# Performance work log

Measured on AMD Instinct MI355X. Metric: run time of the kernel, lower is better.

## Reference

```python
import jax, jax.numpy as jnp
import numpy as np

HEADS = 16
EPS = 1e-5

def _ln(t):
    # LayerNorm over last axis, no affine params
    mu = jnp.mean(t, axis=-1, keepdims=True)
    var = jnp.var(t, axis=-1, keepdims=True)
    return (t - mu) / jnp.sqrt(var + EPS)

def setup_inputs() -> dict:
    key = jax.random.key(0)
    ks = jax.random.split(key, 8)
    b, n, dim, mlp_dim = 4, 2048, 1024, 4096
    s = lambda d: 1.0 / np.sqrt(d)
    return {
        "x": jax.random.normal(ks[0], (b, n, dim), dtype=jnp.float32),
        "Wqkv": jax.random.uniform(ks[1], (dim, 3 * dim), jnp.float32, -s(dim), s(dim)),
        "W1": jax.random.uniform(ks[2], (dim, mlp_dim), jnp.float32, -s(dim), s(dim)),
        "b1": jax.random.uniform(ks[3], (mlp_dim,), jnp.float32, -s(dim), s(dim)),
        "W2": jax.random.uniform(ks[4], (mlp_dim, dim), jnp.float32, -s(mlp_dim), s(mlp_dim)),
        "b2": jax.random.uniform(ks[5], (dim,), jnp.float32, -s(mlp_dim), s(mlp_dim)),
        "Wout": jax.random.uniform(ks[6], (dim, dim), jnp.float32, -s(dim), s(dim)),
        "bout": jax.random.uniform(ks[7], (dim,), jnp.float32, -s(dim), s(dim)),
    }

def reference(x, Wqkv, W1, b1, W2, b2, Wout, bout):
    b, n, dim = x.shape
    h = HEADS
    d = dim // h
    scale = dim ** (-0.5)  # NOTE: module scales by full dim, not head_dim
    qkv = x @ Wqkv  # [b, n, 3*dim]
    qkv = qkv.reshape(b, n, 3, h, d).transpose(2, 0, 3, 1, 4)  # [3, b, h, n, d]
    q, k, v = qkv[0], qkv[1], qkv[2]
    q, k = _ln(q), _ln(k)
    dots = jnp.einsum('bhid,bhjd->bhij', q, k) * scale
    attn = jax.nn.softmax(dots, axis=-1)
    attn_v = jnp.einsum('bhij,bhjd->bhid', attn, v)
    attn_v = attn_v.transpose(0, 2, 1, 3).reshape(b, n, dim)
    attn_out = attn_v @ Wout + bout
    parallel = jax.nn.gelu(x @ W1 + b1, approximate=False) @ W2 + b2
    return _ln(attn_out + parallel)
```

## Files before the change

### kernel.cpp

```cpp
#include <hip/hip_runtime.h>

typedef __attribute__((ext_vector_type(8))) short s16x8;
typedef __attribute__((ext_vector_type(4))) short s16x4;
typedef __attribute__((ext_vector_type(4))) float f32x4;
typedef __attribute__((ext_vector_type(16))) float f32x16;
typedef __attribute__((ext_vector_type(2))) unsigned uint2v;

#define DEVINL __device__ __forceinline__

DEVINL float b2f(short u){ return __uint_as_float(((unsigned)(unsigned short)u) << 16); }
DEVINL short f2bf(float f){
  unsigned u = __float_as_uint(f);
  u += 0x7fffu + ((u >> 16) & 1u);
  return (short)(u >> 16);
}
DEVINL unsigned cvtpk(float lo, float hi){
  unsigned r;
  asm("v_cvt_pk_bf16_f32 %0, %1, %2" : "=v"(r) : "v"(lo), "v"(hi));
  return r;
}
DEVINL float max3f(float a, float b, float c){
  float r; asm("v_max3_f32 %0, %1, %2, %3" : "=v"(r) : "v"(a), "v"(b), "v"(c)); return r;
}

#if __has_builtin(__builtin_amdgcn_exp2f)
#define EXP2F __builtin_amdgcn_exp2f
#else
#define EXP2F exp2f
#endif

DEVINL f32x4 mfma32(s16x8 a, s16x8 b, f32x4 c){
  return __builtin_amdgcn_mfma_f32_16x16x32_bf16(a, b, c, 0, 0, 0);
}
DEVINL f32x16 mfma3216(s16x8 a, s16x8 b, f32x16 c){
  return __builtin_amdgcn_mfma_f32_32x32x16_bf16(a, b, c, 0, 0, 0);
}

DEVINL uint2v pl32swap(unsigned a, unsigned b){
#if __has_builtin(__builtin_amdgcn_permlane32_swap)
  return __builtin_amdgcn_permlane32_swap(a, b, false, false);
#else
  asm volatile("v_permlane32_swap_b32 %0, %1" : "+v"(a), "+v"(b));
  uint2v r; r[0] = a; r[1] = b; return r;
#endif
}

typedef const unsigned __attribute__((address_space(1)))* gas1;
typedef unsigned __attribute__((address_space(3)))* las3;
DEVINL void gload16(const short* g, short* l){
  __builtin_amdgcn_global_load_lds((gas1)g, (las3)l, 16, 0, 0);
}

#define CFENCE asm volatile("" ::: "memory")
#define PBAR  do{ CFENCE; __builtin_amdgcn_sched_barrier(0); __builtin_amdgcn_s_barrier(); \
                  __builtin_amdgcn_sched_barrier(0); CFENCE; }while(0)
#define VMW8 asm volatile("s_waitcnt vmcnt(8)" ::: "memory")
#define VMW4 asm volatile("s_waitcnt vmcnt(4)" ::: "memory")
#define VMW0 asm volatile("s_waitcnt vmcnt(0)" ::: "memory")
#define PRIO1 __builtin_amdgcn_s_setprio(1)
#define PRIO0 __builtin_amdgcn_s_setprio(0)

static const int Bc   = 4;
static const int Nc   = 2048;
static const int DIM  = 1024;
static const int Tc   = Bc * Nc;
static const int MLP  = 4096;
static const int D3   = 3072;

static const size_t OFF_XB    = 0;
static const size_t OFF_WQKVT = OFF_XB    + 16777216;
static const size_t OFF_W1T   = OFF_WQKVT + 6291456;
static const size_t OFF_W2T   = OFF_W1T   + 8388608;
static const size_t OFF_WOUTT = OFF_W2T   + 8388608;
static const size_t OFF_QKV   = OFF_WOUTT + 2097152;
static const size_t OFF_QLN   = OFF_QKV   + 50331648;
static const size_t OFF_KLN   = OFF_QLN   + 16777216;
static const size_t OFF_VT    = OFF_KLN   + 16777216;
static const size_t OFF_ATTNV = OFF_VT    + 16777216;
static const size_t OFF_H     = OFF_QKV;
static const size_t OFF_S2    = OFF_KLN;

DEVINL void transp_body(const float* __restrict__ W, short* __restrict__ Wt,
                        int K, int N, int bid){
  __shared__ float tile[32][33];
  int ntx = N >> 5;
  int tx = bid % ntx, ty = bid / ntx;
  int r = threadIdx.x >> 3, c = (threadIdx.x & 7) * 4;
  f32x4 v = *(const f32x4*)(W + (size_t)(ty*32 + r)*N + tx*32 + c);
  tile[r][c] = v[0]; tile[r][c+1] = v[1]; tile[r][c+2] = v[2]; tile[r][c+3] = v[3];
  __syncthreads();
  s16x4 o;
#pragma unroll
  for (int j = 0; j < 4; ++j) o[j] = f2bf(tile[c+j][r]);
  *(s16x4*)(Wt + (size_t)(tx*32 + r)*K + ty*32 + c) = o;
}

__global__ __launch_bounds__(256) void prep_all(const float* __restrict__ x, short* __restrict__ xb,
                                                const float* __restrict__ Wqkv, short* __restrict__ wqkvt,
                                                const float* __restrict__ W1, short* __restrict__ w1t,
                                                const float* __restrict__ W2, short* __restrict__ w2t,
                                                const float* __restrict__ Wout, short* __restrict__ woutt){
  const int b = blockIdx.x;
  if (b < 4096){
    size_t i = ((size_t)b * 256 + threadIdx.x) * 8;
    f32x4 v0 = *(const f32x4*)(x + i);
    f32x4 v1 = *(const f32x4*)(x + i + 4);
    s16x8 o;
#pragma unroll
    for (int j = 0; j < 4; ++j){ o[j] = f2bf(v0[j]); o[4+j] = f2bf(v1[j]); }
    *(s16x8*)(xb + i) = o;
  } else if (b < 7168){
    transp_body(Wqkv, wqkvt, DIM, D3, b - 4096);
  } else if (b < 11264){
    transp_body(W1, w1t, DIM, MLP, b - 7168);
  } else if (b < 15360){
    transp_body(W2, w2t, MLP, DIM, b - 11264);
  } else {
    transp_body(Wout, woutt, DIM, DIM, b - 15360);
  }
}

template<int ACT, int FUSED, int QKVEPI>
__global__ __launch_bounds__(256, 2) void gemmCF(const short* __restrict__ A, const short* __restrict__ A2,
                                                 const short* __restrict__ Bt, const short* __restrict__ Bt2,
                                                 short* __restrict__ C,
                                                 const float* __restrict__ bias, const float* __restrict__ bias2,
                                                 int M, int N, int K1, int K2,
                                                 short* __restrict__ qln, short* __restrict__ kln,
                                                 short* __restrict__ vtb){
  __shared__ short lds[32768];

  const int tid = threadIdx.x;
  const int w = tid >> 6, lane = tid & 63;
  const int lr = lane & 15, g = lane >> 4;
  const int wr = w >> 1, wc = w & 1;
  const int NT1 = K1 >> 6;
  const int NT = NT1 + (FUSED ? (K2 >> 6) : 0);
  const int NIT = NT >> 1;

  const int nbn = N >> 7;
  const int cpx = gridDim.x >> 3;
  const int bid = (int)blockIdx.x;
  const int sw = (bid & 7)*cpx + (bid >> 3);
  const int nbn8 = nbn >> 3;
  const int T8 = sw >> 6, t64 = sw & 63;
  const int bm = (T8 / nbn8)*8 + (t64 >> 3);
  const int bn = (T8 % nbn8)*8 + (t64 & 7);

  const int l2 = lane >> 2;
  const int gsw = ((lane & 3) - ((lane >> 3) & 3)) & 3;
  const int cof = gsw * 8;
  const int qsw8 = ((g + (lr >> 1)) & 3) * 8;

  const short* ap0h = A  + (size_t)(bm*128 + w*16 + l2)*K1 + cof;
  const short* bp0h = Bt + (size_t)(bn*128 + w*16 + l2)*K1 + cof;
  const short* ap0a = FUSED ? (A2  + (size_t)(bm*128 + w*16 + l2)*K2 + cof) : nullptr;
  const short* bp0a = FUSED ? (Bt2 + (size_t)(bn*128 + w*16 + l2)*K2 + cof) : nullptr;

  auto stA = [&](int s, int T_, int kk){
    short* d0 = lds + s*4096 + w*512;
    if (FUSED && T_ >= NT1){
      size_t off = (size_t)(T_ - NT1)*64 + kk*32;
      gload16(ap0a + off, d0);
      gload16(ap0a + (size_t)64*K2 + off, d0 + 2048);
    } else {
      size_t off = (size_t)T_*64 + kk*32;
      gload16(ap0h + off, d0);
      gload16(ap0h + (size_t)64*K1 + off, d0 + 2048);
    }
  };
  auto stB = [&](int s, int T_, int kk){
    short* d0 = lds + 16384 + s*4096 + w*512;
    if (FUSED && T_ >= NT1){
      size_t off = (size_t)(T_ - NT1)*64 + kk*32;
      gload16(bp0a + off, d0);
      gload16(bp0a + (size_t)64*K2 + off, d0 + 2048);
    } else {
      size_t off = (size_t)T_*64 + kk*32;
      gload16(bp0h + off, d0);
      gload16(bp0h + (size_t)64*K1 + off, d0 + 2048);
    }
  };

#define LDA(s, mi) (*(const s16x8*)&lds[(s)*4096 + (wr*64 + (mi)*16 + lr)*32 + qsw8])
#define LDB(s, ni) (*(const s16x8*)&lds[16384 + (s)*4096 + (wc*64 + (ni)*16 + lr)*32 + qsw8])

  f32x4 acc[4][4] = {};
#define MM(ai, r) \
  acc[r][0]=mfma32(ai,b0,acc[r][0]); acc[r][1]=mfma32(ai,b1,acc[r][1]); \
  acc[r][2]=mfma32(ai,b2,acc[r][2]); acc[r][3]=mfma32(ai,b3,acc[r][3]);
#define RD(s) s16x8 a0=LDA(s,0),a1=LDA(s,1),a2=LDA(s,2),a3=LDA(s,3), \
                    b0=LDB(s,0),b1=LDB(s,1),b2=LDB(s,2),b3=LDB(s,3);
#define MM16 MM(a0,0) MM(a1,1) MM(a2,2) MM(a3,3)

  stA(0,0,0); stB(0,0,0);
  stA(1,0,1); stB(1,0,1);
  stA(2,1,0); stB(2,1,0);
  VMW8;
  PBAR;

  for (int i = 0; i < NIT; ++i){
    const int t = i << 1;
    const bool more = (i + 1 < NIT);
    {
      RD(0)
      stA(3, t+1, 1); stB(3, t+1, 1);
      PBAR; PRIO1; MM16 PRIO0;
      VMW8;
      PBAR;
    }
    {
      RD(1)
      if (more){ stA(0, t+2, 0); stB(0, t+2, 0); }
      PBAR; PRIO1; MM16 PRIO0;
      if (more){ VMW8; } else { VMW4; }
      PBAR;
    }
    {
      RD(2)
      if (more){ stA(1, t+2, 1); stB(1, t+2, 1); }
      PBAR; PRIO1; MM16 PRIO0;
      if (more){ VMW8; } else { VMW0; }
      PBAR;
    }
    {
      RD(3)
      if (more){ stA(2, t+3, 0); stB(2, t+3, 0); }
      PBAR; PRIO1; MM16 PRIO0;
      if (more){ VMW8; }
      PBAR;
    }
  }
#undef MM
#undef RD
#undef MM16
#undef LDA
#undef LDB

  if constexpr (QKVEPI){
#pragma unroll
    for (int a = 0; a < 4; ++a){
#pragma unroll
      for (int ni = 0; ni < 4; ++ni){
        const int col = wc*64 + ni*16 + lr;
        f32x4 v = acc[a][ni];
#pragma unroll
        for (int ii = 0; ii < 4; ++ii)
          lds[(wr*64 + a*16 + 4*g + ii)*130 + col] = f2bf(v[ii]);
      }
    }
    __syncthreads();
    const int part = (bn*128) >> 10;
    const int h0 = ((bn*128) & 1023) >> 6;
    const int rg = bm*128;
    const int b = rg >> 11;
    const int tok0 = rg & 2047;

    if (part < 2){
      short* dstbase = part ? kln : qln;
      const float sc = part ? 1.f : 0.04508422003f;
      const int row = tid >> 1, grp = tid & 1;
      const short* src = &lds[row*130 + grp*64];
      float s = 0.f, sq = 0.f;
#pragma unroll
      for (int i2 = 0; i2 < 8; ++i2){
        s16x8 u = *(const s16x8*)(src + i2*8);
#pragma unroll
        for (int j = 0; j < 8; ++j){ float fv = b2f(u[j]); s += fv; sq += fv*fv; }
      }
      const float mu = s * (1.f/64.f);
      const float var = sq * (1.f/64.f) - mu*mu;
      const float inv = rsqrtf(var + 1e-5f) * sc;
      const int bh = b*16 + h0 + grp;
      short* dst = dstbase + ((size_t)bh*Nc + tok0 + row)*64;
#pragma unroll
      for (int i2 = 0; i2 < 8; ++i2){
        s16x8 u = *(const s16x8*)(src + i2*8);
        s16x8 o;
#pragma unroll
        for (int j = 0; j < 8; ++j) o[j] = f2bf((b2f(u[j]) - mu) * inv);
        *(s16x8*)(dst + i2*8) = o;
      }
    } else {
      const int d = tid & 63, hh = (tid >> 6) & 1, half = tid >> 7;
      const int bh = b*16 + h0 + hh;
      short* dst = vtb + ((size_t)bh*64 + d)*Nc + tok0 + half*64;
#pragma unroll
      for (int i2 = 0; i2 < 8; ++i2){
        s16x8 o;
#pragma unroll
        for (int j = 0; j < 8; ++j)
          o[j] = lds[(half*64 + i2*8 + j)*130 + hh*64 + d];
        *(s16x8*)(dst + i2*8) = o;
      }
    }
    return;
  }

#pragma unroll
  for (int a = 0; a < 4; ++a){
#pragma unroll
    for (int ni = 0; ni < 4; ++ni){
      const int col = wc*64 + ni*16 + lr;
      float bv = bias ? bias[bn*128 + col] : 0.f;
      if (FUSED && bias2) bv += bias2[bn*128 + col];
      f32x4 v = acc[a][ni];
#pragma unroll
      for (int ii = 0; ii < 4; ++ii){
        float val = v[ii] + bv;
        if constexpr (ACT) val = 0.5f*val*(1.f + erff(val*0.70710678118f));
        lds[(wr*64 + a*16 + 4*g + ii)*128 + col] = f2bf(val);
      }
    }
  }
  __syncthreads();
  const size_t crow0 = (size_t)bm * 128;
  const int ch = (tid & 15) * 8;
#pragma unroll
  for (int p = 0; p < 8; ++p){
    const int row = p*16 + (tid >> 4);
    *(s16x8*)&C[(crow0 + row)*N + bn*128 + ch] = *(const s16x8*)&lds[row*128 + ch];
  }
}

__global__ __launch_bounds__(256) void attn_kern(const short* __restrict__ qln, const short* __restrict__ kln,
                                                 const short* __restrict__ vtb, short* __restrict__ attnv){
  __shared__ short Ks[2][64*72];
  __shared__ short Vs[2][64*72];
  const int tid = threadIdx.x;
  const int bh = blockIdx.x >> 4, qt = blockIdx.x & 15;
  const int b = bh >> 4, h = bh & 15;
  const int w = tid >> 6, lane = tid & 63;
  const int lq = lane & 31, hi = lane >> 5;
  const int qrow = qt*128 + w*32 + lq;

  const short* qp = qln + ((size_t)bh*Nc + qrow)*64 + hi*8;
  s16x8 qf[4];
#pragma unroll
  for (int m = 0; m < 4; ++m) qf[m] = *(const s16x8*)(qp + m*16);

  f32x16 o0 = {0,0,0,0,0,0,0,0,0,0,0,0,0,0,0,0};
  f32x16 o1 = {0,0,0,0,0,0,0,0,0,0,0,0,0,0,0,0};
  float mrun = -INFINITY, l = 0.f;

  const int sr = tid >> 3;
  const int sc = (tid & 7) * 8;
  const short* kb0 = kln + (size_t)bh*Nc*64;
  const short* vb0 = vtb + (size_t)bh*64*Nc;

  s16x8 kr0, kr1, vr0, vr1;
  {
    kr0 = *(const s16x8*)(kb0 + (size_t)sr*64 + sc);
    kr1 = *(const s16x8*)(kb0 + (size_t)(32 + sr)*64 + sc);
    vr0 = *(const s16x8*)(vb0 + (size_t)sr*Nc + sc);
    vr1 = *(const s16x8*)(vb0 + (size_t)(32 + sr)*Nc + sc);
  }

  for (int kt = 0; kt < 32; ++kt){
    const int cur = kt & 1;
    *(s16x8*)&Ks[cur][sr*72 + sc]        = kr0;
    *(s16x8*)&Ks[cur][(32 + sr)*72 + sc] = kr1;
    *(s16x8*)&Vs[cur][sr*72 + sc]        = vr0;
    *(s16x8*)&Vs[cur][(32 + sr)*72 + sc] = vr1;
    __syncthreads();
    if (kt + 1 < 32){
      const short* kb = kb0 + (size_t)(kt+1)*64*64;
      const short* vb = vb0 + (kt+1)*64;
      kr0 = *(const s16x8*)(kb + (size_t)sr*64 + sc);
      kr1 = *(const s16x8*)(kb + (size_t)(32 + sr)*64 + sc);
      vr0 = *(const s16x8*)(vb + (size_t)sr*Nc + sc);
      vr1 = *(const s16x8*)(vb + (size_t)(32 + sr)*Nc + sc);
    }

    f32x16 st0 = {0,0,0,0,0,0,0,0,0,0,0,0,0,0,0,0};
    f32x16 st1 = {0,0,0,0,0,0,0,0,0,0,0,0,0,0,0,0};
#pragma unroll
    for (int m = 0; m < 4; ++m){
      s16x8 kf0 = *(const s16x8*)&Ks[cur][ lq      *72 + m*16 + hi*8];
      s16x8 kf1 = *(const s16x8*)&Ks[cur][(32 + lq)*72 + m*16 + hi*8];
      st0 = mfma3216(kf0, qf[m], st0);
      st1 = mfma3216(kf1, qf[m], st1);
    }

    float cmax = max3f(st0[0], st0[1], st0[2]);
    cmax = max3f(cmax, st0[3], st0[4]);   cmax = max3f(cmax, st0[5], st0[6]);
    cmax = max3f(cmax, st0[7], st0[8]);   cmax = max3f(cmax, st0[9], st0[10]);
    cmax = max3f(cmax, st0[11], st0[12]); cmax = max3f(cmax, st0[13], st0[14]);
    cmax = max3f(cmax, st0[15], st1[0]);  cmax = max3f(cmax, st1[1], st1[2]);
    cmax = max3f(cmax, st1[3], st1[4]);   cmax = max3f(cmax, st1[5], st1[6]);
    cmax = max3f(cmax, st1[7], st1[8]);   cmax = max3f(cmax, st1[9], st1[10]);
    cmax = max3f(cmax, st1[11], st1[12]); cmax = max3f(cmax, st1[13], st1[14]);
    cmax = fmaxf(cmax, st1[15]);
    cmax = fmaxf(cmax, __shfl_xor(cmax, 32));
    if (__any(cmax > mrun + 8.f)){
      float mnew = fmaxf(mrun, cmax);
      float fr = EXP2F(mrun - mnew);
      l *= fr;
#pragma unroll
      for (int r = 0; r < 16; ++r){ o0[r] *= fr; o1[r] *= fr; }
      mrun = mnew;
    }
    float p0[16], p1[16];
#pragma unroll
    for (int r = 0; r < 16; ++r){
      p0[r] = EXP2F(st0[r] - mrun); l += p0[r];
      p1[r] = EXP2F(st1[r] - mrun); l += p1[r];
    }

#pragma unroll
    for (int kc = 0; kc < 2; ++kc){
      const float* p = kc ? p1 : p0;
#pragma unroll
      for (int kh = 0; kh < 2; ++kh){
        int r0 = kh*8;
        unsigned wa = cvtpk(p[r0+0], p[r0+1]);
        unsigned wb = cvtpk(p[r0+4], p[r0+5]);
        unsigned wc2 = cvtpk(p[r0+2], p[r0+3]);
        unsigned wd = cvtpk(p[r0+6], p[r0+7]);
        uint2v s1 = pl32swap(wa, wb);
        uint2v s2 = pl32swap(wc2, wd);
        union { unsigned u[4]; s16x8 v; } pu;
        pu.u[0] = s1[0]; pu.u[1] = s2[0]; pu.u[2] = s1[1]; pu.u[3] = s2[1];
        s16x8 vf0 = *(const s16x8*)&Vs[cur][ lq      *72 + kc*32 + kh*16 + hi*8];
        s16x8 vf1 = *(const s16x8*)&Vs[cur][(32 + lq)*72 + kc*32 + kh*16 + hi*8];
        o0 = mfma3216(vf0, pu.v, o0);
        o1 = mfma3216(vf1, pu.v, o1);
      }
    }
  }

  l += __shfl_xor(l, 32);
  float inv = 1.f / l;
  short* orow = attnv + ((size_t)(b*Nc + qrow))*DIM + h*64;
#pragma unroll
  for (int r = 0; r < 16; r += 2){
    int dv = (r&3) + 8*(r>>2) + 4*hi;
    *(unsigned*)&orow[dv]      = cvtpk(o0[r]*inv, o0[r+1]*inv);
    *(unsigned*)&orow[32 + dv] = cvtpk(o1[r]*inv, o1[r+1]*inv);
  }
}

__global__ __launch_bounds__(256) void final_ln(const short* __restrict__ s2, float* __restrict__ out){
  __shared__ float red[16];
  int row = blockIdx.x, tid = threadIdx.x;
  size_t base = (size_t)row*DIM + tid*4;
  s16x4 a = *(const s16x4*)(s2 + base);
  float v[4]; float s = 0.f, sq = 0.f;
#pragma unroll
  for (int i = 0; i < 4; ++i){ v[i] = b2f(a[i]); s += v[i]; sq += v[i]*v[i]; }
#pragma unroll
  for (int m = 1; m < 64; m <<= 1){ s += __shfl_xor(s, m); sq += __shfl_xor(sq, m); }
  int wv = tid >> 6;
  if ((tid & 63) == 0){ red[wv] = s; red[8 + wv] = sq; }
  __syncthreads();
  if (tid == 0){
    float S = red[0] + red[1] + red[2] + red[3];
    float Q = red[8] + red[9] + red[10] + red[11];
    float mu = S * (1.f/1024.f);
    float var = Q * (1.f/1024.f) - mu*mu;
    red[12] = mu; red[13] = rsqrtf(var + 1e-5f);
  }
  __syncthreads();
  float mu = red[12], inv = red[13];
#pragma unroll
  for (int i = 0; i < 4; ++i) out[base + i] = (v[i] - mu) * inv;
}

extern "C" void kernel_launch(void* const* d_in, const int* in_sizes, int n_in,
                              void* d_out, int out_size, void* d_ws, size_t ws_size,
                              hipStream_t stream){
  const float* x    = (const float*)d_in[0];
  const float* Wqkv = (const float*)d_in[1];
  const float* W1   = (const float*)d_in[2];
  const float* b1   = (const float*)d_in[3];
  const float* W2   = (const float*)d_in[4];
  const float* b2   = (const float*)d_in[5];
  const float* Wout = (const float*)d_in[6];
  const float* bout = (const float*)d_in[7];
  float* out = (float*)d_out;
  char* ws = (char*)d_ws;

  short* xb    = (short*)(ws + OFF_XB);
  short* wqkvt = (short*)(ws + OFF_WQKVT);
  short* w1t   = (short*)(ws + OFF_W1T);
  short* w2t   = (short*)(ws + OFF_W2T);
  short* woutt = (short*)(ws + OFF_WOUTT);
  short* qln   = (short*)(ws + OFF_QLN);
  short* kln   = (short*)(ws + OFF_KLN);
  short* vtb   = (short*)(ws + OFF_VT);
  short* attnv = (short*)(ws + OFF_ATTNV);
  short* hbuf  = (short*)(ws + OFF_H);
  short* s2    = (short*)(ws + OFF_S2);

  prep_all<<<16384, 256, 0, stream>>>(x, xb, Wqkv, wqkvt, W1, w1t, W2, w2t, Wout, woutt);

  gemmCF<0,0,1><<<(Tc/128)*(D3/128), 256, 0, stream>>>(xb, xb, wqkvt, wqkvt, nullptr,
                                                       nullptr, nullptr, Tc, D3, DIM, DIM,
                                                       qln, kln, vtb);
  attn_kern<<<64*16, 256, 0, stream>>>(qln, kln, vtb, attnv);

  gemmCF<1,0,0><<<(Tc/128)*(MLP/128), 256, 0, stream>>>(xb, xb, w1t, w1t, hbuf,
                                                        b1, nullptr, Tc, MLP, DIM, DIM,
                                                        nullptr, nullptr, nullptr);
  gemmCF<0,1,0><<<(Tc/128)*(DIM/128), 256, 0, stream>>>(hbuf, attnv, w2t, woutt, s2,
                                                        b2, bout, Tc, DIM, MLP, DIM,
                                                        nullptr, nullptr, nullptr);

  final_ln<<<Tc, 256, 0, stream>>>(s2, out);
}
```

Measured before the change: 405.7 us.

## Co-schedule attention and MLP-up GEMM in one launch; compact workspace

Attention and the GELU MLP-up GEMM now run as one horizontally fused kernel, with block IDs below 1024 doing attention and the rest doing a specialised GEMM body. The aim is to fill the GPU, since attention alone launches only 1024 blocks, and to overlap its latency-bound work with the compute-bound GEMM. The weight prep is split in two so the W2 and Wout transposes run after the fused kernel, which lets the workspace be aliased more tightly. The risks are tail imbalance between the two block types, the attention blocks being held to the GEMM's larger LDS allocation and launch bounds, and aliasing errors in the new buffer offsets.

```diff
diff --git a/kernel.cpp b/kernel.cpp
--- a/kernel.cpp
+++ b/kernel.cpp
@@ -68,17 +68,16 @@
 static const int D3   = 3072;
 
 static const size_t OFF_XB    = 0;
-static const size_t OFF_WQKVT = OFF_XB    + 16777216;
-static const size_t OFF_W1T   = OFF_WQKVT + 6291456;
-static const size_t OFF_W2T   = OFF_W1T   + 8388608;
-static const size_t OFF_WOUTT = OFF_W2T   + 8388608;
-static const size_t OFF_QKV   = OFF_WOUTT + 2097152;
-static const size_t OFF_QLN   = OFF_QKV   + 50331648;
-static const size_t OFF_KLN   = OFF_QLN   + 16777216;
-static const size_t OFF_VT    = OFF_KLN   + 16777216;
-static const size_t OFF_ATTNV = OFF_VT    + 16777216;
-static const size_t OFF_H     = OFF_QKV;
-static const size_t OFF_S2    = OFF_KLN;
+static const size_t OFF_W1T   = 16777216;
+static const size_t OFF_QLN   = 25165824;
+static const size_t OFF_KLN   = 41943040;
+static const size_t OFF_VT    = 58720256;
+static const size_t OFF_ATTNV = 75497472;
+static const size_t OFF_HB    = 92274688;
+static const size_t OFF_WQKVT = OFF_HB;
+static const size_t OFF_W2T   = 0;
+static const size_t OFF_WOUTT = 8388608;
+static const size_t OFF_S2    = OFF_QLN;
 
 DEVINL void transp_body(const float* __restrict__ W, short* __restrict__ Wt,
                         int K, int N, int bid){
@@ -95,11 +94,9 @@
   *(s16x4*)(Wt + (size_t)(tx*32 + r)*K + ty*32 + c) = o;
 }
 
-__global__ __launch_bounds__(256) void prep_all(const float* __restrict__ x, short* __restrict__ xb,
-                                                const float* __restrict__ Wqkv, short* __restrict__ wqkvt,
-                                                const float* __restrict__ W1, short* __restrict__ w1t,
-                                                const float* __restrict__ W2, short* __restrict__ w2t,
-                                                const float* __restrict__ Wout, short* __restrict__ woutt){
+__global__ __launch_bounds__(256) void prep1(const float* __restrict__ x, short* __restrict__ xb,
+                                             const float* __restrict__ Wqkv, short* __restrict__ wqkvt,
+                                             const float* __restrict__ W1, short* __restrict__ w1t){
   const int b = blockIdx.x;
   if (b < 4096){
     size_t i = ((size_t)b * 256 + threadIdx.x) * 8;
@@ -111,13 +108,16 @@
     *(s16x8*)(xb + i) = o;
   } else if (b < 7168){
     transp_body(Wqkv, wqkvt, DIM, D3, b - 4096);
-  } else if (b < 11264){
+  } else {
     transp_body(W1, w1t, DIM, MLP, b - 7168);
-  } else if (b < 15360){
-    transp_body(W2, w2t, MLP, DIM, b - 11264);
-  } else {
-    transp_body(Wout, woutt, DIM, DIM, b - 15360);
-  }
+  }
+}
+
+__global__ __launch_bounds__(256) void prep2(const float* __restrict__ W2, short* __restrict__ w2t,
+                                             const float* __restrict__ Wout, short* __restrict__ woutt){
+  const int b = blockIdx.x;
+  if (b < 4096) transp_body(W2, w2t, MLP, DIM, b);
+  else          transp_body(Wout, woutt, DIM, DIM, b - 4096);
 }
 
 template<int ACT, int FUSED, int QKVEPI>
@@ -323,12 +323,13 @@
   }
 }
 
-__global__ __launch_bounds__(256) void attn_kern(const short* __restrict__ qln, const short* __restrict__ kln,
-                                                 const short* __restrict__ vtb, short* __restrict__ attnv){
-  __shared__ short Ks[2][64*72];
-  __shared__ short Vs[2][64*72];
+DEVINL void attn_body(int bid, short* smem,
+                      const short* __restrict__ qln, const short* __restrict__ kln,
+                      const short* __restrict__ vtb, short* __restrict__ attnv){
+  short* Ks = smem;
+  short* Vs = smem + 9216;
   const int tid = threadIdx.x;
-  const int bh = blockIdx.x >> 4, qt = blockIdx.x & 15;
+  const int bh = bid >> 4, qt = bid & 15;
   const int b = bh >> 4, h = bh & 15;
   const int w = tid >> 6, lane = tid & 63;
   const int lq = lane & 31, hi = lane >> 5;
@@ -358,10 +359,10 @@
 
   for (int kt = 0; kt < 32; ++kt){
     const int cur = kt & 1;
-    *(s16x8*)&Ks[cur][sr*72 + sc]        = kr0;
-    *(s16x8*)&Ks[cur][(32 + sr)*72 + sc] = kr1;
-    *(s16x8*)&Vs[cur][sr*72 + sc]        = vr0;
-    *(s16x8*)&Vs[cur][(32 + sr)*72 + sc] = vr1;
+    *(s16x8*)&Ks[cur*4608 + sr*72 + sc]        = kr0;
+    *(s16x8*)&Ks[cur*4608 + (32 + sr)*72 + sc] = kr1;
+    *(s16x8*)&Vs[cur*4608 + sr*72 + sc]        = vr0;
+    *(s16x8*)&Vs[cur*4608 + (32 + sr)*72 + sc] = vr1;
     __syncthreads();
     if (kt + 1 < 32){
       const short* kb = kb0 + (size_t)(kt+1)*64*64;
@@ -376,8 +377,8 @@
     f32x16 st1 = {0,0,0,0,0,0,0,0,0,0,0,0,0,0,0,0};
 #pragma unroll
     for (int m = 0; m < 4; ++m){
-      s16x8 kf0 = *(const s16x8*)&Ks[cur][ lq      *72 + m*16 + hi*8];
-      s16x8 kf1 = *(const s16x8*)&Ks[cur][(32 + lq)*72 + m*16 + hi*8];
+      s16x8 kf0 = *(const s16x8*)&Ks[cur*4608 +  lq      *72 + m*16 + hi*8];
+      s16x8 kf1 = *(const s16x8*)&Ks[cur*4608 + (32 + lq)*72 + m*16 + hi*8];
       st0 = mfma3216(kf0, qf[m], st0);
       st1 = mfma3216(kf1, qf[m], st1);
     }
@@ -421,8 +422,8 @@
         uint2v s2 = pl32swap(wc2, wd);
         union { unsigned u[4]; s16x8 v; } pu;
         pu.u[0] = s1[0]; pu.u[1] = s2[0]; pu.u[2] = s1[1]; pu.u[3] = s2[1];
-        s16x8 vf0 = *(const s16x8*)&Vs[cur][ lq      *72 + kc*32 + kh*16 + hi*8];
-        s16x8 vf1 = *(const s16x8*)&Vs[cur][(32 + lq)*72 + kc*32 + kh*16 + hi*8];
+        s16x8 vf0 = *(const s16x8*)&Vs[cur*4608 +  lq      *72 + kc*32 + kh*16 + hi*8];
+        s16x8 vf1 = *(const s16x8*)&Vs[cur*4608 + (32 + lq)*72 + kc*32 + kh*16 + hi*8];
         o0 = mfma3216(vf0, pu.v, o0);
         o1 = mfma3216(vf1, pu.v, o1);
       }
@@ -437,6 +438,138 @@
     int dv = (r&3) + 8*(r>>2) + 4*hi;
     *(unsigned*)&orow[dv]      = cvtpk(o0[r]*inv, o0[r+1]*inv);
     *(unsigned*)&orow[32 + dv] = cvtpk(o1[r]*inv, o1[r+1]*inv);
+  }
+}
+
+DEVINL void mlp1_body(int bid, short* lds,
+                      const short* __restrict__ A, const short* __restrict__ Bt,
+                      short* __restrict__ C, const float* __restrict__ bias){
+  const int N = MLP, K1 = DIM;
+  const int tid = threadIdx.x;
+  const int w = tid >> 6, lane = tid & 63;
+  const int lr = lane & 15, g = lane >> 4;
+  const int wr = w >> 1, wc = w & 1;
+  const int NIT = 8;
+
+  const int nbn = N >> 7;
+  const int cpx = 256;
+  const int sw = (bid & 7)*cpx + (bid >> 3);
+  const int nbn8 = nbn >> 3;
+  const int T8 = sw >> 6, t64 = sw & 63;
+  const int bm = (T8 / nbn8)*8 + (t64 >> 3);
+  const int bn = (T8 % nbn8)*8 + (t64 & 7);
+
+  const int l2 = lane >> 2;
+  const int gsw = ((lane & 3) - ((lane >> 3) & 3)) & 3;
+  const int cof = gsw * 8;
+  const int qsw8 = ((g + (lr >> 1)) & 3) * 8;
+
+  const short* ap0h = A  + (size_t)(bm*128 + w*16 + l2)*K1 + cof;
+  const short* bp0h = Bt + (size_t)(bn*128 + w*16 + l2)*K1 + cof;
+
+  auto stA = [&](int s, int T_, int kk){
+    short* d0 = lds + s*4096 + w*512;
+    size_t off = (size_t)T_*64 + kk*32;
+    gload16(ap0h + off, d0);
+    gload16(ap0h + (size_t)64*K1 + off, d0 + 2048);
+  };
+  auto stB = [&](int s, int T_, int kk){
+    short* d0 = lds + 16384 + s*4096 + w*512;
+    size_t off = (size_t)T_*64 + kk*32;
+    gload16(bp0h + off, d0);
+    gload16(bp0h + (size_t)64*K1 + off, d0 + 2048);
+  };
+
+#define LDA1(s, mi) (*(const s16x8*)&lds[(s)*4096 + (wr*64 + (mi)*16 + lr)*32 + qsw8])
+#define LDB1(s, ni) (*(const s16x8*)&lds[16384 + (s)*4096 + (wc*64 + (ni)*16 + lr)*32 + qsw8])
+
+  f32x4 acc[4][4] = {};
+#define MM1(ai, r) \
+  acc[r][0]=mfma32(ai,b0,acc[r][0]); acc[r][1]=mfma32(ai,b1,acc[r][1]); \
+  acc[r][2]=mfma32(ai,b2,acc[r][2]); acc[r][3]=mfma32(ai,b3,acc[r][3]);
+#define RD1(s) s16x8 a0=LDA1(s,0),a1=LDA1(s,1),a2=LDA1(s,2),a3=LDA1(s,3), \
+                     b0=LDB1(s,0),b1=LDB1(s,1),b2=LDB1(s,2),b3=LDB1(s,3);
+#define MM16_1 MM1(a0,0) MM1(a1,1) MM1(a2,2) MM1(a3,3)
+
+  stA(0,0,0); stB(0,0,0);
+  stA(1,0,1); stB(1,0,1);
+  stA(2,1,0); stB(2,1,0);
+  VMW8;
+  PBAR;
+
+  for (int i = 0; i < NIT; ++i){
+    const int t = i << 1;
+    const bool more = (i + 1 < NIT);
+    {
+      RD1(0)
+      stA(3, t+1, 1); stB(3, t+1, 1);
+      PBAR; PRIO1; MM16_1 PRIO0;
+      VMW8;
+      PBAR;
+    }
+    {
+      RD1(1)
+      if (more){ stA(0, t+2, 0); stB(0, t+2, 0); }
+      PBAR; PRIO1; MM16_1 PRIO0;
+      if (more){ VMW8; } else { VMW4; }
+      PBAR;
+    }
+    {
+      RD1(2)
+      if (more){ stA(1, t+2, 1); stB(1, t+2, 1); }
+      PBAR; PRIO1; MM16_1 PRIO0;
+      if (more){ VMW8; } else { VMW0; }
+      PBAR;
+    }
+    {
+      RD1(3)
+      if (more){ stA(2, t+3, 0); stB(2, t+3, 0); }
+      PBAR; PRIO1; MM16_1 PRIO0;
+      if (more){ VMW8; }
+      PBAR;
+    }
+  }
+#undef MM1
+#undef RD1
+#undef MM16_1
+#undef LDA1
+#undef LDB1
+
+#pragma unroll
+  for (int a = 0; a < 4; ++a){
+#pragma unroll
+    for (int ni = 0; ni < 4; ++ni){
+      const int col = wc*64 + ni*16 + lr;
+      const float bv = bias[bn*128 + col];
+      f32x4 v = acc[a][ni];
+#pragma unroll
+      for (int ii = 0; ii < 4; ++ii){
+        float val = v[ii] + bv;
+        val = 0.5f*val*(1.f + erff(val*0.70710678118f));
+        lds[(wr*64 + a*16 + 4*g + ii)*128 + col] = f2bf(val);
+      }
+    }
+  }
+  __syncthreads();
+  const size_t crow0 = (size_t)bm * 128;
+  const int ch = (tid & 15) * 8;
+#pragma unroll
+  for (int p = 0; p < 8; ++p){
+    const int row = p*16 + (tid >> 4);
+    *(s16x8*)&C[(crow0 + row)*N + bn*128 + ch] = *(const s16x8*)&lds[row*128 + ch];
+  }
+}
+
+__global__ __launch_bounds__(256, 2) void attn_mlp1(const short* __restrict__ qln, const short* __restrict__ kln,
+                                                    const short* __restrict__ vtb, short* __restrict__ attnv,
+                                                    const short* __restrict__ xb, const short* __restrict__ w1t,
+                                                    short* __restrict__ hbuf, const float* __restrict__ b1){
+  __shared__ short smem[32768];
+  const int bid = (int)blockIdx.x;
+  if (bid < 1024){
+    attn_body(bid, smem, qln, kln, vtb, attnv);
+  } else {
+    mlp1_body(bid - 1024, smem, xb, w1t, hbuf, b1);
   }
 }
 
@@ -481,27 +614,27 @@
   char* ws = (char*)d_ws;
 
   short* xb    = (short*)(ws + OFF_XB);
+  short* w1t   = (short*)(ws + OFF_W1T);
   short* wqkvt = (short*)(ws + OFF_WQKVT);
-  short* w1t   = (short*)(ws + OFF_W1T);
-  short* w2t   = (short*)(ws + OFF_W2T);
-  short* woutt = (short*)(ws + OFF_WOUTT);
   short* qln   = (short*)(ws + OFF_QLN);
   short* kln   = (short*)(ws + OFF_KLN);
   short* vtb   = (short*)(ws + OFF_VT);
   short* attnv = (short*)(ws + OFF_ATTNV);
-  short* hbuf  = (short*)(ws + OFF_H);
+  short* hbuf  = (short*)(ws + OFF_HB);
+  short* w2t   = (short*)(ws + OFF_W2T);
+  short* woutt = (short*)(ws + OFF_WOUTT);
   short* s2    = (short*)(ws + OFF_S2);
 
-  prep_all<<<16384, 256, 0, stream>>>(x, xb, Wqkv, wqkvt, W1, w1t, W2, w2t, Wout, woutt);
+  prep1<<<11264, 256, 0, stream>>>(x, xb, Wqkv, wqkvt, W1, w1t);
 
   gemmCF<0,0,1><<<(Tc/128)*(D3/128), 256, 0, stream>>>(xb, xb, wqkvt, wqkvt, nullptr,
                                                        nullptr, nullptr, Tc, D3, DIM, DIM,
                                                        qln, kln, vtb);
-  attn_kern<<<64*16, 256, 0, stream>>>(qln, kln, vtb, attnv);
-
-  gemmCF<1,0,0><<<(Tc/128)*(MLP/128), 256, 0, stream>>>(xb, xb, w1t, w1t, hbuf,
-                                                        b1, nullptr, Tc, MLP, DIM, DIM,
-                                                        nullptr, nullptr, nullptr);
+
+  attn_mlp1<<<1024 + 2048, 256, 0, stream>>>(qln, kln, vtb, attnv, xb, w1t, hbuf, b1);
+
+  prep2<<<5120, 256, 0, stream>>>(W2, w2t, Wout, woutt);
+
   gemmCF<0,1,0><<<(Tc/128)*(DIM/128), 256, 0, stream>>>(hbuf, attnv, w2t, woutt, s2,
                                                         b2, bout, Tc, DIM, MLP, DIM,
                                                         nullptr, nullptr, nullptr);
```

Measured after the change: 377.0 us. 1.08x faster.
